# Kernel optimization log

Hardware: AMD Instinct MI355X
Metric: run time of the kernel (lower is better)

The kernel has to match this reference:

```python
import jax, jax.numpy as jnp
import numpy as np

L = 2        # num stacked decoder layers (len(layer_indexes))
S = 2048     # seq_len (prefill)
H = 2048     # hidden_size
NH = 16      # num_heads == num_key_value_heads
D = 128      # head_dim
I = 5632     # intermediate_size
EPS = 1e-6   # rms_norm_eps
NEG = -1e9   # additive causal mask value


def setup_inputs() -> dict:
    key = jax.random.key(0)
    ks = jax.random.split(key, 10)
    scale = 0.02
    hidden_states = jax.random.normal(ks[0], (1, S, H), jnp.float32)
    # causal additive mask, matching the attention_mask parameter in prefill mode
    attention_mask = jnp.where(jnp.tril(jnp.ones((S, S), bool)), 0.0, NEG)[None, None].astype(jnp.float32)
    position_ids = jnp.arange(S, dtype=jnp.int32)[None]
    # Llama rotary tables: (max_seq, head_dim), cos/sin repeated over both halves
    inv_freq = 1.0 / (10000.0 ** (jnp.arange(0, D, 2, dtype=jnp.float32) / D))
    ang = jnp.arange(S, dtype=jnp.float32)[:, None] * inv_freq[None, :]   # [S, D/2]
    cached_cos = jnp.concatenate([jnp.cos(ang), jnp.cos(ang)], axis=-1)   # [S, D]
    cached_sin = jnp.concatenate([jnp.sin(ang), jnp.sin(ang)], axis=-1)
    wq = jax.random.normal(ks[1], (L, H, H), jnp.float32) * scale
    wk = jax.random.normal(ks[2], (L, H, H), jnp.float32) * scale
    wv = jax.random.normal(ks[3], (L, H, H), jnp.float32) * scale
    wo = jax.random.normal(ks[4], (L, H, H), jnp.float32) * scale
    w_gate = jax.random.normal(ks[5], (L, I, H), jnp.float32) * scale
    w_up = jax.random.normal(ks[6], (L, I, H), jnp.float32) * scale
    w_down = jax.random.normal(ks[7], (L, H, I), jnp.float32) * scale
    ln1 = jnp.ones((L, H), jnp.float32)
    ln2 = jnp.ones((L, H), jnp.float32)
    return {"hidden_states": hidden_states, "attention_mask": attention_mask,
            "cached_cos": cached_cos, "cached_sin": cached_sin,
            "wq": wq, "wk": wk, "wv": wv, "wo": wo,
            "w_gate": w_gate, "w_up": w_up, "w_down": w_down,
            "ln1": ln1, "ln2": ln2, "position_ids": position_ids}


def _rms_norm(x, w):
    # variance = mean(x^2) (no mean subtraction), then scale -- exactly as in build_decoder
    var = jnp.mean(x * x, axis=-1, keepdims=True)
    return (x / jnp.sqrt(var + EPS)) * w


def _rotate_half(x):
    x1, x2 = jnp.split(x, 2, axis=-1)
    return jnp.concatenate([-x2, x1], axis=-1)


def _rope(x, cos, sin):
    return x * cos + _rotate_half(x) * sin


def _forward(hidden_states, attention_mask, cached_cos, cached_sin,
             wq, wk, wv, wo, w_gate, w_up, w_down, ln1, ln2, position_ids):
    pos = position_ids[0]                              # [S]
    cos = cached_cos[pos][None, None]                  # [1,1,S,D]
    sin = cached_sin[pos][None, None]
    inv_sqrt_d = 1.0 / np.sqrt(D).astype(np.float32)
    x = hidden_states                                  # [1,S,H]
    for i in range(L):
        h = _rms_norm(x, ln1[i])
        q = (h @ wq[i].T).reshape(1, S, NH, D).transpose(0, 2, 1, 3)  # [1,NH,S,D]
        k = (h @ wk[i].T).reshape(1, S, NH, D).transpose(0, 2, 1, 3)
        v = (h @ wv[i].T).reshape(1, S, NH, D).transpose(0, 2, 1, 3)
        q = _rope(q, cos, sin)
        k = _rope(k, cos, sin)
        scores = jnp.einsum('bhqd,bhkd->bhqk', q, k) * inv_sqrt_d + attention_mask
        attn = jax.nn.softmax(scores, axis=-1)
        o = jnp.einsum('bhqk,bhkd->bhqd', attn, v)
        o = o.transpose(0, 2, 1, 3).reshape(1, S, H)
        x = x + o @ wo[i].T
        h = _rms_norm(x, ln2[i])
        mlp = (jax.nn.silu(h @ w_gate[i].T) * (h @ w_up[i].T)) @ w_down[i].T
        x = x + mlp
    return x


def reference(hidden_states, attention_mask, cached_cos, cached_sin,
              wq, wk, wv, wo, w_gate, w_up, w_down, ln1, ln2, position_ids):
    return _forward(hidden_states, attention_mask, cached_cos, cached_sin,
                    wq, wk, wv, wo, w_gate, w_up, w_down, ln1, ln2, position_ids)
```

## Files before the change

kernel.cpp:

```cpp
#include <hip/hip_runtime.h>
#include <hip/hip_bf16.h>

constexpr int kL = 2;
constexpr int kS = 2048;
constexpr int kH = 2048;
constexpr int kNH = 16;
constexpr int kD = 128;
constexpr int kI = 5632;

using s16x8 = __attribute__((ext_vector_type(8))) short;
using s16x4 = __attribute__((ext_vector_type(4))) short;
using f32x4 = __attribute__((ext_vector_type(4))) float;

__device__ __forceinline__ float b2f(short s) {
  union { unsigned u; float f; } v;
  v.u = ((unsigned)(unsigned short)s) << 16;
  return v.f;
}
__device__ __forceinline__ short f2bs(float f) {
  __hip_bfloat16 h = __float2bfloat16(f);
  union { __hip_bfloat16 h; short s; } u;
  u.h = h;
  return u.s;
}

__device__ __forceinline__ void lds16(const void* g, void* l) {
  __builtin_amdgcn_global_load_lds(
      (const __attribute__((address_space(1))) void*)g,
      (__attribute__((address_space(3))) void*)l, 16, 0, 0);
}

__device__ __forceinline__ void swz_block(int gx, int& bx, int& by) {
  const int gy = gridDim.y;
  const int lin = by * gx + bx;
  if ((gx & 3) == 0 && (gy & 1) == 0) {
    const int cx = gx >> 2, cy = gy >> 1;
    const int xcd = lin & 7;
    const int s = lin >> 3;
    bx = (xcd & 3) * cx + s % cx;
    by = (xcd >> 2) * cy + s / cx;
  } else if (((gx * gy) & 7) == 0) {
    const int cpx = (gx * gy) >> 3;
    const int l2 = (lin & 7) * cpx + (lin >> 3);
    bx = l2 % gx;
    by = l2 / gx;
  }
}

__global__ __launch_bounds__(256) void cvt_w(const float* __restrict__ in,
                                             short* __restrict__ outp, int n8) {
  for (int i = blockIdx.x * blockDim.x + threadIdx.x; i < n8; i += gridDim.x * blockDim.x) {
    const float4 a = ((const float4*)in)[2 * i];
    const float4 b = ((const float4*)in)[2 * i + 1];
    s16x8 o;
    o[0] = f2bs(a.x); o[1] = f2bs(a.y); o[2] = f2bs(a.z); o[3] = f2bs(a.w);
    o[4] = f2bs(b.x); o[5] = f2bs(b.y); o[6] = f2bs(b.z); o[7] = f2bs(b.w);
    ((s16x8*)outp)[i] = o;
  }
}

template <int EPI>
__global__ __launch_bounds__(256) void gemm_db(const short* __restrict__ A,
                                               const short* __restrict__ B,
                                               short* __restrict__ C0,
                                               short* __restrict__ C1,
                                               short* __restrict__ C2,
                                               float* __restrict__ Cf,
                                               int M, int N, int K) {
  __shared__ short As0[128 * 64], Bs0[128 * 64];
  __shared__ short As1[128 * 64], Bs1[128 * 64];
  const int t = threadIdx.x;
  const int lane = t & 63, wid = t >> 6;
  int bx = blockIdx.x, by = blockIdx.y;
  swz_block(gridDim.x, bx, by);
  const int m0 = by * 128, n0 = bx * 128;
  const int wr = (wid >> 1) * 64, wc = (wid & 1) * 64;
  const int fr = lane & 15, g4 = lane >> 4;

  const int srow = (lane >> 3);
  const int scol = (((lane & 7) << 4) ^ (srow << 4)) >> 1;

  f32x4 acc[4][4] = {};

  auto stage = [&](short* Ad, short* Bd, int k0) {
    #pragma unroll
    for (int c = 0; c < 4; ++c) {
      const int chunk = wid * 4 + c;
      const int e0 = chunk * 512;
      const int row = chunk * 8 + srow;
      lds16(A + (size_t)(m0 + row) * K + k0 + scol, Ad + e0);
      lds16(B + (size_t)(n0 + row) * K + k0 + scol, Bd + e0);
    }
  };

  auto compute = [&](const short* Xs, const short* Ys) {
    #pragma unroll
    for (int ks = 0; ks < 2; ++ks) {
      s16x8 a[4], b[4];
      #pragma unroll
      for (int m = 0; m < 4; ++m) {
        const int r = wr + m * 16 + fr;
        a[m] = *(const s16x8*)&Xs[r * 64 + (((ks * 4 + g4) ^ (r & 7)) << 3)];
      }
      #pragma unroll
      for (int n = 0; n < 4; ++n) {
        const int r = wc + n * 16 + fr;
        b[n] = *(const s16x8*)&Ys[r * 64 + (((ks * 4 + g4) ^ (r & 7)) << 3)];
      }
      #pragma unroll
      for (int m = 0; m < 4; ++m)
        #pragma unroll
        for (int n = 0; n < 4; ++n)
          acc[m][n] = __builtin_amdgcn_mfma_f32_16x16x32_bf16(a[m], b[n], acc[m][n], 0, 0, 0);
    }
  };

  const int nt = K >> 6;
  stage(As0, Bs0, 0);
  __syncthreads();
  for (int tt = 0; tt < nt; tt += 2) {
    stage(As1, Bs1, (tt + 1) << 6);
    compute(As0, Bs0);
    __syncthreads();
    if (tt + 2 < nt) stage(As0, Bs0, (tt + 2) << 6);
    compute(As1, Bs1);
    __syncthreads();
  }

  #pragma unroll
  for (int m = 0; m < 4; ++m) {
    #pragma unroll
    for (int n = 0; n < 4; ++n) {
      const int rb = m0 + wr + m * 16 + g4 * 4;
      const int col = n0 + wc + n * 16 + fr;
      if (EPI == 0) {
        #pragma unroll
        for (int j = 0; j < 4; ++j)
          C0[(size_t)(rb + j) * N + col] = f2bs(acc[m][n][j]);
      } else if (EPI == 1) {
        #pragma unroll
        for (int j = 0; j < 4; ++j)
          Cf[(size_t)(rb + j) * N + col] += acc[m][n][j];
      } else if (EPI == 2) {
        s16x4 pk;
        #pragma unroll
        for (int j = 0; j < 4; ++j) pk[j] = f2bs(acc[m][n][j]);
        *(s16x4*)&C0[(size_t)col * M + rb] = pk;
      } else if (EPI == 3) {
        const int seg = n0 >> 11;
        const int cl = col - (seg << 11);
        if (seg == 0) {
          #pragma unroll
          for (int j = 0; j < 4; ++j) C0[(size_t)(rb + j) * 2048 + cl] = f2bs(acc[m][n][j]);
        } else if (seg == 1) {
          #pragma unroll
          for (int j = 0; j < 4; ++j) C1[(size_t)(rb + j) * 2048 + cl] = f2bs(acc[m][n][j]);
        } else {
          s16x4 pk;
          #pragma unroll
          for (int j = 0; j < 4; ++j) pk[j] = f2bs(acc[m][n][j]);
          *(s16x4*)&C2[(size_t)cl * M + rb] = pk;
        }
      } else {
        const bool useg = (n0 >= 5632);
        const int cl = col - (useg ? 5632 : 0);
        short* dst = useg ? C1 : C0;
        #pragma unroll
        for (int j = 0; j < 4; ++j) dst[(size_t)(rb + j) * 5632 + cl] = f2bs(acc[m][n][j]);
      }
    }
  }
}

template <int EPI>
__global__ __launch_bounds__(256) void gemm_btf(const short* __restrict__ A,
                                                const float* __restrict__ B,
                                                short* __restrict__ Cb,
                                                float* __restrict__ Cf,
                                                int M, int N, int K) {
  __shared__ short As[128 * 32];
  __shared__ short Bs[128 * 32];
  const int t = threadIdx.x;
  const int lane = t & 63, wid = t >> 6;
  int bx = blockIdx.x, by = blockIdx.y;
  swz_block(gridDim.x, bx, by);
  const int m0 = by * 128, n0 = bx * 128;
  const int wr = (wid >> 1) * 64, wc = (wid & 1) * 64;
  const int fr = lane & 15, h8 = (lane >> 4) * 8;
  const int brow = t >> 1, bcol = (t & 1) * 16;
  const float* bsrc = B + (size_t)(n0 + brow) * K + bcol;

  f32x4 acc[4][4] = {};

  for (int k0 = 0; k0 < K; k0 += 32) {
    const float4 bv0 = *(const float4*)(bsrc + k0);
    const float4 bv1 = *(const float4*)(bsrc + k0 + 4);
    const float4 bv2 = *(const float4*)(bsrc + k0 + 8);
    const float4 bv3 = *(const float4*)(bsrc + k0 + 12);
    __syncthreads();
    {
      const float bf[16] = {bv0.x, bv0.y, bv0.z, bv0.w, bv1.x, bv1.y, bv1.z, bv1.w,
                            bv2.x, bv2.y, bv2.z, bv2.w, bv3.x, bv3.y, bv3.z, bv3.w};
      s16x8 wlo, whi;
      #pragma unroll
      for (int j = 0; j < 8; ++j) { wlo[j] = f2bs(bf[j]); whi[j] = f2bs(bf[8 + j]); }
      *(s16x8*)&Bs[brow * 32 + bcol] = wlo;
      *(s16x8*)&Bs[brow * 32 + bcol + 8] = whi;
    }
    #pragma unroll
    for (int c = 0; c < 2; ++c) {
      const int e0 = c * 2048 + wid * 512;
      const int e = e0 + lane * 8;
      const int row = e >> 5, col = e & 31;
      lds16(A + (size_t)(m0 + row) * K + k0 + col, (void*)(As + e0));
    }
    __syncthreads();

    s16x8 a[4], b[4];
    #pragma unroll
    for (int m = 0; m < 4; ++m) a[m] = *(const s16x8*)&As[(wr + m * 16 + fr) * 32 + h8];
    #pragma unroll
    for (int n = 0; n < 4; ++n) b[n] = *(const s16x8*)&Bs[(wc + n * 16 + fr) * 32 + h8];
    #pragma unroll
    for (int m = 0; m < 4; ++m)
      #pragma unroll
      for (int n = 0; n < 4; ++n)
        acc[m][n] = __builtin_amdgcn_mfma_f32_16x16x32_bf16(a[m], b[n], acc[m][n], 0, 0, 0);
  }

  const int g4 = lane >> 4;
  #pragma unroll
  for (int m = 0; m < 4; ++m) {
    #pragma unroll
    for (int n = 0; n < 4; ++n) {
      const int rb = m0 + wr + m * 16 + g4 * 4;
      const int col = n0 + wc + n * 16 + fr;
      if (EPI == 0) {
        #pragma unroll
        for (int j = 0; j < 4; ++j)
          Cb[(size_t)(rb + j) * N + col] = f2bs(acc[m][n][j]);
      } else if (EPI == 1) {
        #pragma unroll
        for (int j = 0; j < 4; ++j)
          Cf[(size_t)(rb + j) * N + col] += acc[m][n][j];
      } else {
        s16x4 pk;
        #pragma unroll
        for (int j = 0; j < 4; ++j) pk[j] = f2bs(acc[m][n][j]);
        *(s16x4*)&Cb[(size_t)col * M + rb] = pk;
      }
    }
  }
}

__global__ __launch_bounds__(256) void rmsnorm_k(const float* __restrict__ x,
                                                 const float* __restrict__ w,
                                                 short* __restrict__ h) {
  const int row = blockIdx.x, t = threadIdx.x;
  const float4* xr = (const float4*)(x + (size_t)row * kH);
  const float4 v0 = xr[2 * t], v1 = xr[2 * t + 1];
  float ss = v0.x * v0.x + v0.y * v0.y + v0.z * v0.z + v0.w * v0.w +
             v1.x * v1.x + v1.y * v1.y + v1.z * v1.z + v1.w * v1.w;
  #pragma unroll
  for (int off = 1; off < 64; off <<= 1) ss += __shfl_xor(ss, off);
  __shared__ float red[4];
  if ((t & 63) == 0) red[t >> 6] = ss;
  __syncthreads();
  ss = red[0] + red[1] + red[2] + red[3];
  const float rs = rsqrtf(ss * (1.0f / kH) + 1e-6f);
  const float4 w0 = ((const float4*)w)[2 * t];
  const float4 w1 = ((const float4*)w)[2 * t + 1];
  const float xv[8] = {v0.x, v0.y, v0.z, v0.w, v1.x, v1.y, v1.z, v1.w};
  const float wv[8] = {w0.x, w0.y, w0.z, w0.w, w1.x, w1.y, w1.z, w1.w};
  s16x8 o;
  #pragma unroll
  for (int j = 0; j < 8; ++j) o[j] = f2bs(xv[j] * rs * wv[j]);
  *(s16x8*)&h[(size_t)row * kH + t * 8] = o;
}

__global__ __launch_bounds__(256) void rope_k(short* __restrict__ q, short* __restrict__ k,
                                              const float* __restrict__ cosb,
                                              const float* __restrict__ sinb,
                                              const int* __restrict__ pos) {
  const int s = blockIdx.x;
  const int p = pos[s];
  const size_t rowb = (size_t)s * kH;
  for (int idx = threadIdx.x; idx < kNH * 64; idx += 256) {
    const int hh = idx >> 6, d = idx & 63;
    const float c = cosb[p * kD + d];
    const float sn = sinb[p * kD + d];
    const size_t i1 = rowb + hh * kD + d, i2 = i1 + 64;
    const float q1 = b2f(q[i1]), q2 = b2f(q[i2]);
    q[i1] = f2bs(q1 * c - q2 * sn);
    q[i2] = f2bs(q2 * c + q1 * sn);
    const float k1 = b2f(k[i1]), k2 = b2f(k[i2]);
    k[i1] = f2bs(k1 * c - k2 * sn);
    k[i2] = f2bs(k2 * c + k1 * sn);
  }
}

__global__ __launch_bounds__(256) void attn_k(const short* __restrict__ q,
                                              const short* __restrict__ k,
                                              const short* __restrict__ vt,
                                              short* __restrict__ o) {
  __shared__ short Kl[64 * 128];
  __shared__ short Vl[128 * 64];
  __shared__ short Pl[4][16 * 72];
  const int h = blockIdx.x;
  const int qi = blockIdx.y;
  const int t = threadIdx.x;
  const int lane = t & 63, wid = t >> 6;
  const int fr = lane & 15, g4 = lane >> 4;
  const int q0 = qi * 64 + wid * 16;

  s16x8 aq[4];
  {
    const short* qp = q + (size_t)(q0 + fr) * kH + h * kD;
    #pragma unroll
    for (int ks = 0; ks < 4; ++ks) aq[ks] = *(const s16x8*)(qp + ks * 32 + g4 * 8);
  }
  f32x4 acco[8] = {};
  float mrun[4], lrun[4];
  #pragma unroll
  for (int j = 0; j < 4; ++j) { mrun[j] = -3.0e30f; lrun[j] = 0.f; }

  for (int tt = 0; tt <= qi; ++tt) {
    const int kv0 = tt * 64;
    __syncthreads();
    #pragma unroll
    for (int c = 0; c < 4; ++c) {
      const int b = c * 4096 + t * 16;
      {
        const int row = b >> 8, ch = b & 255;
        const s16x8 kvl =
            *(const s16x8*)(k + (size_t)(kv0 + row) * kH + h * kD + (ch >> 1));
        *(s16x8*)((char*)Kl + row * 256 + (ch ^ ((row & 7) << 4))) = kvl;
      }
      {
        const int dd = b >> 7, ch = b & 127;
        const s16x8 vvl =
            *(const s16x8*)(vt + (size_t)(h * kD + dd) * kS + kv0 + (ch >> 1));
        *(s16x8*)((char*)Vl + dd * 128 + (ch ^ ((dd & 7) << 4))) = vvl;
      }
    }
    __syncthreads();

    f32x4 sc[4] = {};
    #pragma unroll
    for (int ks = 0; ks < 4; ++ks) {
      const int ch16 = ks * 4 + g4;
      #pragma unroll
      for (int nf = 0; nf < 4; ++nf) {
        const int row = nf * 16 + fr;
        const s16x8 bk =
            *(const s16x8*)((const char*)Kl + row * 256 + ((ch16 ^ (row & 7)) << 4));
        sc[nf] = __builtin_amdgcn_mfma_f32_16x16x32_bf16(aq[ks], bk, sc[nf], 0, 0, 0);
      }
    }

    float val[4][4];
    #pragma unroll
    for (int nf = 0; nf < 4; ++nf) {
      #pragma unroll
      for (int j = 0; j < 4; ++j) {
        float v = sc[nf][j] * 0.08838834764831845f;
        if (tt == qi) {
          const int colg = kv0 + nf * 16 + fr;
          const int rowg = q0 + g4 * 4 + j;
          if (colg > rowg) v -= 1.0e9f;
        }
        val[nf][j] = v;
      }
    }

    #pragma unroll
    for (int j = 0; j < 4; ++j) {
      float rm = fmaxf(fmaxf(val[0][j], val[1][j]), fmaxf(val[2][j], val[3][j]));
      rm = fmaxf(rm, __shfl_xor(rm, 1));
      rm = fmaxf(rm, __shfl_xor(rm, 2));
      rm = fmaxf(rm, __shfl_xor(rm, 4));
      rm = fmaxf(rm, __shfl_xor(rm, 8));
      const float mnew = fmaxf(mrun[j], rm);
      const float corr = __expf(mrun[j] - mnew);
      mrun[j] = mnew;
      float ps = 0.f;
      #pragma unroll
      for (int nf = 0; nf < 4; ++nf) {
        const float p = __expf(val[nf][j] - mnew);
        ps += p;
        Pl[wid][(g4 * 4 + j) * 72 + nf * 16 + fr] = f2bs(p);
      }
      ps += __shfl_xor(ps, 1);
      ps += __shfl_xor(ps, 2);
      ps += __shfl_xor(ps, 4);
      ps += __shfl_xor(ps, 8);
      lrun[j] = lrun[j] * corr + ps;
      #pragma unroll
      for (int nf = 0; nf < 8; ++nf) acco[nf][j] *= corr;
    }

    #pragma unroll
    for (int ks = 0; ks < 2; ++ks) {
      const s16x8 ap = *(const s16x8*)(&Pl[wid][fr * 72 + ks * 32 + g4 * 8]);
      const int ch16 = ks * 4 + g4;
      #pragma unroll
      for (int nf = 0; nf < 8; ++nf) {
        const int dd = nf * 16 + fr;
        const s16x8 bv =
            *(const s16x8*)((const char*)Vl + dd * 128 + ((ch16 ^ (dd & 7)) << 4));
        acco[nf] = __builtin_amdgcn_mfma_f32_16x16x32_bf16(ap, bv, acco[nf], 0, 0, 0);
      }
    }
  }

  #pragma unroll
  for (int nf = 0; nf < 8; ++nf) {
    #pragma unroll
    for (int j = 0; j < 4; ++j) {
      const int rowg = q0 + g4 * 4 + j;
      o[(size_t)rowg * kH + h * kD + nf * 16 + fr] = f2bs(acco[nf][j] / lrun[j]);
    }
  }
}

__global__ void silu_mul(short* __restrict__ g, const short* __restrict__ u, int n8) {
  for (int i = blockIdx.x * blockDim.x + threadIdx.x; i < n8; i += gridDim.x * blockDim.x) {
    const s16x8 gv = ((const s16x8*)g)[i];
    const s16x8 uv = ((const s16x8*)u)[i];
    s16x8 o;
    #pragma unroll
    for (int j = 0; j < 8; ++j) {
      const float gf = b2f(gv[j]);
      const float s = gf / (1.f + __expf(-gf));
      o[j] = f2bs(s * b2f(uv[j]));
    }
    ((s16x8*)g)[i] = o;
  }
}

extern "C" void kernel_launch(void* const* d_in, const int* in_sizes, int n_in,
                              void* d_out, int out_size, void* d_ws, size_t ws_size,
                              hipStream_t stream) {
  (void)in_sizes; (void)n_in; (void)out_size;
  const float* hidden = (const float*)d_in[0];
  const float* cosb = (const float*)d_in[2];
  const float* sinb = (const float*)d_in[3];
  const float* wq = (const float*)d_in[4];
  const float* wk = (const float*)d_in[5];
  const float* wv = (const float*)d_in[6];
  const float* wo = (const float*)d_in[7];
  const float* wg = (const float*)d_in[8];
  const float* wu = (const float*)d_in[9];
  const float* wd = (const float*)d_in[10];
  const float* ln1 = (const float*)d_in[11];
  const float* ln2 = (const float*)d_in[12];
  const int* pos = (const int*)d_in[13];
  float* out = (float*)d_out;

  char* p = (char*)d_ws;
  float* x  = (float*)p;  p += (size_t)kS * kH * 4;
  short* hb = (short*)p;  p += (size_t)kS * kH * 2;
  char* U = p;            p += (size_t)kS * kI * 4;
  short* qb = (short*)(U);
  short* kb = (short*)(U + (size_t)kS * kH * 2);
  short* vtb = (short*)(U + (size_t)kS * kH * 4);
  short* ob = (short*)(U + (size_t)kS * kH * 6);
  short* gb = (short*)(U);
  short* ub = (short*)(U + (size_t)kS * kI * 2);
  short* wbuf = (short*)p;
  const size_t nHH = (size_t)kH * kH, nIH = (size_t)kI * kH;
  const size_t need = (size_t)(p - (char*)d_ws) + (4 * nHH + 3 * nIH) * 2;
  const bool pre = ws_size >= need;

  short* wqb = wbuf;
  short* wkb = wqb + nHH;
  short* wvb = wkb + nHH;
  short* wob = wvb + nHH;
  short* wgb = wob + nHH;
  short* wub = wgb + nIH;
  short* wdb = wub + nIH;

  hipMemcpyAsync(x, hidden, (size_t)kS * kH * 4, hipMemcpyDeviceToDevice, stream);
  for (int l = 0; l < kL; ++l) {
    rmsnorm_k<<<kS, 256, 0, stream>>>(x, ln1 + (size_t)l * kH, hb);
    if (pre) {
      cvt_w<<<2048, 256, 0, stream>>>(wq + l * nHH, wqb, (int)(nHH / 8));
      cvt_w<<<2048, 256, 0, stream>>>(wk + l * nHH, wkb, (int)(nHH / 8));
      cvt_w<<<2048, 256, 0, stream>>>(wv + l * nHH, wvb, (int)(nHH / 8));
      cvt_w<<<2048, 256, 0, stream>>>(wo + l * nHH, wob, (int)(nHH / 8));
      cvt_w<<<2048, 256, 0, stream>>>(wg + l * nIH, wgb, (int)(nIH / 8));
      cvt_w<<<2048, 256, 0, stream>>>(wu + l * nIH, wub, (int)(nIH / 8));
      cvt_w<<<2048, 256, 0, stream>>>(wd + l * nIH, wdb, (int)(nIH / 8));
      gemm_db<3><<<dim3(6144 / 128, kS / 128), 256, 0, stream>>>(
          hb, wqb, qb, kb, vtb, nullptr, kS, 6144, kH);
      rope_k<<<kS, 256, 0, stream>>>(qb, kb, cosb, sinb, pos);
      attn_k<<<dim3(kNH, kS / 64), 256, 0, stream>>>(qb, kb, vtb, ob);
      gemm_db<1><<<dim3(kH / 128, kS / 128), 256, 0, stream>>>(
          ob, wob, nullptr, nullptr, nullptr, x, kS, kH, kH);
      rmsnorm_k<<<kS, 256, 0, stream>>>(x, ln2 + (size_t)l * kH, hb);
      gemm_db<4><<<dim3(11264 / 128, kS / 128), 256, 0, stream>>>(
          hb, wgb, gb, ub, nullptr, nullptr, kS, 11264, kH);
      silu_mul<<<1408, 256, 0, stream>>>(gb, ub, kS * kI / 8);
      gemm_db<1><<<dim3(kH / 128, kS / 128), 256, 0, stream>>>(
          gb, wdb, nullptr, nullptr, nullptr, x, kS, kH, kI);
    } else {
      gemm_btf<0><<<dim3(kH / 128, kS / 128), 256, 0, stream>>>(hb, wq + l * nHH, qb, nullptr, kS, kH, kH);
      gemm_btf<0><<<dim3(kH / 128, kS / 128), 256, 0, stream>>>(hb, wk + l * nHH, kb, nullptr, kS, kH, kH);
      gemm_btf<2><<<dim3(kH / 128, kS / 128), 256, 0, stream>>>(hb, wv + l * nHH, vtb, nullptr, kS, kH, kH);
      rope_k<<<kS, 256, 0, stream>>>(qb, kb, cosb, sinb, pos);
      attn_k<<<dim3(kNH, kS / 64), 256, 0, stream>>>(qb, kb, vtb, ob);
      gemm_btf<1><<<dim3(kH / 128, kS / 128), 256, 0, stream>>>(ob, wo + l * nHH, nullptr, x, kS, kH, kH);
      rmsnorm_k<<<kS, 256, 0, stream>>>(x, ln2 + (size_t)l * kH, hb);
      gemm_btf<0><<<dim3(kI / 128, kS / 128), 256, 0, stream>>>(hb, wg + l * nIH, gb, nullptr, kS, kI, kH);
      gemm_btf<0><<<dim3(kI / 128, kS / 128), 256, 0, stream>>>(hb, wu + l * nIH, ub, nullptr, kS, kI, kH);
      silu_mul<<<1408, 256, 0, stream>>>(gb, ub, kS * kI / 8);
      gemm_btf<1><<<dim3(kH / 128, kS / 128), 256, 0, stream>>>(gb, wd + l * nIH, nullptr, x, kS, kH, kI);
    }
  }
  hipMemcpyAsync(out, x, (size_t)kS * kH * 4, hipMemcpyDeviceToDevice, stream);
}
```

Baseline: 987.4 us.

## Double-buffer attention K/V tiles, fuse weight conversions, set MFMA priority

The attention kernel now prefetches the next K/V tile into registers while the current tile is computed, and writes it into a second LDS buffer afterwards, so one barrier per iteration replaces two. The seven per-layer weight conversion launches are merged into a single kernel writing into contiguous buffers, and unused GEMM epilogues are removed. s_setprio is raised around the MFMA sections. The trade-off is doubled LDS for K/V plus extra registers, which can reduce attention occupancy.

```diff
diff --git a/kernel.cpp b/kernel.cpp
--- a/kernel.cpp
+++ b/kernel.cpp
@@ -47,15 +47,36 @@
   }
 }
 
-__global__ __launch_bounds__(256) void cvt_w(const float* __restrict__ in,
-                                             short* __restrict__ outp, int n8) {
-  for (int i = blockIdx.x * blockDim.x + threadIdx.x; i < n8; i += gridDim.x * blockDim.x) {
-    const float4 a = ((const float4*)in)[2 * i];
-    const float4 b = ((const float4*)in)[2 * i + 1];
-    s16x8 o;
-    o[0] = f2bs(a.x); o[1] = f2bs(a.y); o[2] = f2bs(a.z); o[3] = f2bs(a.w);
-    o[4] = f2bs(b.x); o[5] = f2bs(b.y); o[6] = f2bs(b.z); o[7] = f2bs(b.w);
-    ((s16x8*)outp)[i] = o;
+__global__ __launch_bounds__(256) void cvt_all(const float* __restrict__ q,
+                                               const float* __restrict__ k,
+                                               const float* __restrict__ v,
+                                               const float* __restrict__ o,
+                                               const float* __restrict__ g,
+                                               const float* __restrict__ u,
+                                               const float* __restrict__ d,
+                                               short* __restrict__ dst) {
+  constexpr int HH8 = (kH * kH) / 8;
+  constexpr int IH8 = (kI * kH) / 8;
+  constexpr int tot = 4 * HH8 + 3 * IH8;
+  for (int i = blockIdx.x * blockDim.x + threadIdx.x; i < tot; i += gridDim.x * blockDim.x) {
+    const float* src;
+    int off;
+    if (i < 4 * HH8) {
+      const int s = i >> 19;
+      off = i & (HH8 - 1);
+      src = s == 0 ? q : s == 1 ? k : s == 2 ? v : o;
+    } else {
+      const int j = i - 4 * HH8;
+      const int s = j / IH8;
+      off = j - s * IH8;
+      src = s == 0 ? g : s == 1 ? u : d;
+    }
+    const float4 a = ((const float4*)src)[2 * off];
+    const float4 b = ((const float4*)src)[2 * off + 1];
+    s16x8 ov;
+    ov[0] = f2bs(a.x); ov[1] = f2bs(a.y); ov[2] = f2bs(a.z); ov[3] = f2bs(a.w);
+    ov[4] = f2bs(b.x); ov[5] = f2bs(b.y); ov[6] = f2bs(b.z); ov[7] = f2bs(b.w);
+    ((s16x8*)dst)[i] = ov;
   }
 }
 
@@ -133,19 +154,10 @@
     for (int n = 0; n < 4; ++n) {
       const int rb = m0 + wr + m * 16 + g4 * 4;
       const int col = n0 + wc + n * 16 + fr;
-      if (EPI == 0) {
-        #pragma unroll
-        for (int j = 0; j < 4; ++j)
-          C0[(size_t)(rb + j) * N + col] = f2bs(acc[m][n][j]);
-      } else if (EPI == 1) {
+      if (EPI == 1) {
         #pragma unroll
         for (int j = 0; j < 4; ++j)
           Cf[(size_t)(rb + j) * N + col] += acc[m][n][j];
-      } else if (EPI == 2) {
-        s16x4 pk;
-        #pragma unroll
-        for (int j = 0; j < 4; ++j) pk[j] = f2bs(acc[m][n][j]);
-        *(s16x4*)&C0[(size_t)col * M + rb] = pk;
       } else if (EPI == 3) {
         const int seg = n0 >> 11;
         const int cl = col - (seg << 11);
@@ -303,8 +315,8 @@
                                               const short* __restrict__ k,
                                               const short* __restrict__ vt,
                                               short* __restrict__ o) {
-  __shared__ short Kl[64 * 128];
-  __shared__ short Vl[128 * 64];
+  __shared__ short Kl[2][64 * 128];
+  __shared__ short Vl[2][128 * 64];
   __shared__ short Pl[4][16 * 72];
   const int h = blockIdx.x;
   const int qi = blockIdx.y;
@@ -324,28 +336,38 @@
   #pragma unroll
   for (int j = 0; j < 4; ++j) { mrun[j] = -3.0e30f; lrun[j] = 0.f; }
 
+  s16x8 kreg[4], vreg[4];
+  auto loadt = [&](int tt) {
+    const int kv0 = tt * 64;
+    #pragma unroll
+    for (int c = 0; c < 4; ++c) {
+      const int b = c * 4096 + t * 16;
+      kreg[c] = *(const s16x8*)(k + (size_t)(kv0 + (b >> 8)) * kH + h * kD + ((b & 255) >> 1));
+      vreg[c] = *(const s16x8*)(vt + (size_t)(h * kD + (b >> 7)) * kS + kv0 + ((b & 127) >> 1));
+    }
+  };
+  auto writet = [&](int buf) {
+    #pragma unroll
+    for (int c = 0; c < 4; ++c) {
+      const int b = c * 4096 + t * 16;
+      const int kr = b >> 8, kc = b & 255;
+      *(s16x8*)((char*)Kl[buf] + kr * 256 + (kc ^ ((kr & 7) << 4))) = kreg[c];
+      const int vr = b >> 7, vc = b & 127;
+      *(s16x8*)((char*)Vl[buf] + vr * 128 + (vc ^ ((vr & 7) << 4))) = vreg[c];
+    }
+  };
+
+  loadt(0);
+  writet(0);
+  __syncthreads();
+
   for (int tt = 0; tt <= qi; ++tt) {
     const int kv0 = tt * 64;
-    __syncthreads();
-    #pragma unroll
-    for (int c = 0; c < 4; ++c) {
-      const int b = c * 4096 + t * 16;
-      {
-        const int row = b >> 8, ch = b & 255;
-        const s16x8 kvl =
-            *(const s16x8*)(k + (size_t)(kv0 + row) * kH + h * kD + (ch >> 1));
-        *(s16x8*)((char*)Kl + row * 256 + (ch ^ ((row & 7) << 4))) = kvl;
-      }
-      {
-        const int dd = b >> 7, ch = b & 127;
-        const s16x8 vvl =
-            *(const s16x8*)(vt + (size_t)(h * kD + dd) * kS + kv0 + (ch >> 1));
-        *(s16x8*)((char*)Vl + dd * 128 + (ch ^ ((dd & 7) << 4))) = vvl;
-      }
-    }
-    __syncthreads();
+    const int cur = tt & 1;
+    if (tt < qi) loadt(tt + 1);
 
     f32x4 sc[4] = {};
+    __builtin_amdgcn_s_setprio(1);
     #pragma unroll
     for (int ks = 0; ks < 4; ++ks) {
       const int ch16 = ks * 4 + g4;
@@ -353,10 +375,11 @@
       for (int nf = 0; nf < 4; ++nf) {
         const int row = nf * 16 + fr;
         const s16x8 bk =
-            *(const s16x8*)((const char*)Kl + row * 256 + ((ch16 ^ (row & 7)) << 4));
+            *(const s16x8*)((const char*)Kl[cur] + row * 256 + ((ch16 ^ (row & 7)) << 4));
         sc[nf] = __builtin_amdgcn_mfma_f32_16x16x32_bf16(aq[ks], bk, sc[nf], 0, 0, 0);
       }
     }
+    __builtin_amdgcn_s_setprio(0);
 
     float val[4][4];
     #pragma unroll
@@ -399,6 +422,7 @@
       for (int nf = 0; nf < 8; ++nf) acco[nf][j] *= corr;
     }
 
+    __builtin_amdgcn_s_setprio(1);
     #pragma unroll
     for (int ks = 0; ks < 2; ++ks) {
       const s16x8 ap = *(const s16x8*)(&Pl[wid][fr * 72 + ks * 32 + g4 * 8]);
@@ -407,10 +431,14 @@
       for (int nf = 0; nf < 8; ++nf) {
         const int dd = nf * 16 + fr;
         const s16x8 bv =
-            *(const s16x8*)((const char*)Vl + dd * 128 + ((ch16 ^ (dd & 7)) << 4));
+            *(const s16x8*)((const char*)Vl[cur] + dd * 128 + ((ch16 ^ (dd & 7)) << 4));
         acco[nf] = __builtin_amdgcn_mfma_f32_16x16x32_bf16(ap, bv, acco[nf], 0, 0, 0);
       }
     }
+    __builtin_amdgcn_s_setprio(0);
+
+    if (tt < qi) writet(cur ^ 1);
+    __syncthreads();
   }
 
   #pragma unroll
@@ -473,24 +501,17 @@
   const bool pre = ws_size >= need;
 
   short* wqb = wbuf;
-  short* wkb = wqb + nHH;
-  short* wvb = wkb + nHH;
-  short* wob = wvb + nHH;
+  short* wob = wqb + 3 * nHH;
   short* wgb = wob + nHH;
-  short* wub = wgb + nIH;
-  short* wdb = wub + nIH;
+  short* wdb = wgb + 2 * nIH;
 
   hipMemcpyAsync(x, hidden, (size_t)kS * kH * 4, hipMemcpyDeviceToDevice, stream);
   for (int l = 0; l < kL; ++l) {
     rmsnorm_k<<<kS, 256, 0, stream>>>(x, ln1 + (size_t)l * kH, hb);
     if (pre) {
-      cvt_w<<<2048, 256, 0, stream>>>(wq + l * nHH, wqb, (int)(nHH / 8));
-      cvt_w<<<2048, 256, 0, stream>>>(wk + l * nHH, wkb, (int)(nHH / 8));
-      cvt_w<<<2048, 256, 0, stream>>>(wv + l * nHH, wvb, (int)(nHH / 8));
-      cvt_w<<<2048, 256, 0, stream>>>(wo + l * nHH, wob, (int)(nHH / 8));
-      cvt_w<<<2048, 256, 0, stream>>>(wg + l * nIH, wgb, (int)(nIH / 8));
-      cvt_w<<<2048, 256, 0, stream>>>(wu + l * nIH, wub, (int)(nIH / 8));
-      cvt_w<<<2048, 256, 0, stream>>>(wd + l * nIH, wdb, (int)(nIH / 8));
+      cvt_all<<<2048, 256, 0, stream>>>(wq + l * nHH, wk + l * nHH, wv + l * nHH,
+                                        wo + l * nHH, wg + l * nIH, wu + l * nIH,
+                                        wd + l * nIH, wbuf);
       gemm_db<3><<<dim3(6144 / 128, kS / 128), 256, 0, stream>>>(
           hb, wqb, qb, kb, vtb, nullptr, kS, 6144, kH);
       rope_k<<<kS, 256, 0, stream>>>(qb, kb, cosb, sinb, pos);
```

After: 951.4 us. 1.04x faster.
